# Optimization experiments

Hardware: AMD Instinct MI355X
Metric: run time of the kernel (lower is better)

The kernel has to match this reference:

```python
import jax, jax.numpy as jnp
import numpy as np

VOCAB, N_EMBD, BATCH, SEQ = 50257, 768, 8, 1024


def setup_inputs() -> dict:
    key = jax.random.key(0)
    k1, k2, k3, k4, k5 = jax.random.split(key, 5)
    data = jax.random.randint(k1, (BATCH, SEQ), 0, VOCAB, dtype=jnp.int64 if jax.config.jax_enable_x64 else jnp.int32)
    label = jax.random.randint(k2, (BATCH, SEQ), 0, VOCAB, dtype=data.dtype)
    wte = jax.random.normal(k3, (VOCAB, N_EMBD), dtype=jnp.float32) * 0.02
    wpe = jax.random.normal(k4, (SEQ, N_EMBD), dtype=jnp.float32) * 0.02
    W = jax.random.normal(k5, (VOCAB, N_EMBD), dtype=jnp.float32) * 0.02
    return {"data": data, "label": label, "wte": wte, "wpe": wpe, "W": W}


def reference(data, label, wte, wpe, W):
    # token + position embeddings: [B,S,D]
    x = wte[data] + wpe[None, :, :]
    # tanh-approx GELU (matches nn.GELU(approximate='tanh'))
    x = jax.nn.gelu(x, approximate=True)
    # vocab projection (no bias): [B,S,V]
    logits = jnp.einsum('bsd,vd->bsv', x, W)
    logits2d = logits.reshape(BATCH * SEQ, VOCAB)
    labels1d = label.reshape(BATCH * SEQ)
    logp = jax.nn.log_softmax(logits2d, axis=-1)
    nll = -jnp.take_along_axis(logp, labels1d[:, None], axis=-1)[:, 0]
    return jnp.mean(nll)
```

## Files before the change

kernel.cpp:

```cpp
#include <hip/hip_runtime.h>
#include <hip/hip_bf16.h>
#include <cmath>

#define BATCH   8
#define SEQ     1024
#define ROWS    8192
#define DIM     768
#define VOCAB   50257
#define VPAD    50304
#define NVB     393
#define NMB     64

typedef __attribute__((ext_vector_type(8))) short bf16x8;
typedef __attribute__((ext_vector_type(4))) float f32x4;

__device__ __forceinline__ float b2f(ushort u) {
    return __uint_as_float(((unsigned int)u) << 16);
}

__device__ __forceinline__ ushort f2b(float f) {
    unsigned int u = __float_as_uint(f);
    u += 0x7FFFu + ((u >> 16) & 1u);
    return (ushort)(u >> 16);
}

__device__ __forceinline__ float gelu_tanh(float x) {
    const float c = 0.7978845608028654f;
    float t = c * (x + 0.044715f * x * x * x);
    return 0.5f * x * (1.0f + tanhf(t));
}

__device__ __forceinline__ void async16(const void* g, void* l) {
    __builtin_amdgcn_global_load_lds((const __attribute__((address_space(1))) void*)g,
                                     (__attribute__((address_space(3))) void*)l,
                                     16, 0, 0);
}

__global__ void convert_w(const float* __restrict__ W, ushort* __restrict__ Wb) {
    const size_t NQ  = (size_t)VPAD  * DIM / 4;
    const size_t NVQ = (size_t)VOCAB * DIM / 4;
    for (size_t q = (size_t)blockIdx.x * blockDim.x + threadIdx.x; q < NQ;
         q += (size_t)gridDim.x * blockDim.x) {
        ushort4 o;
        if (q < NVQ) {
            float4 f = ((const float4*)W)[q];
            o.x = f2b(f.x); o.y = f2b(f.y); o.z = f2b(f.z); o.w = f2b(f.w);
        } else {
            o.x = 0; o.y = 0; o.z = 0; o.w = 0;
        }
        ((ushort4*)Wb)[q] = o;
    }
}

__global__ void build_x(const int* __restrict__ data, const float* __restrict__ wte,
                        const float* __restrict__ wpe, ushort* __restrict__ Xb) {
    const int row = blockIdx.x;
    const int s   = row & (SEQ - 1);
    const int tok = data[row];
    const int t   = threadIdx.x;
    float4 a = ((const float4*)(wte + (size_t)tok * DIM))[t];
    float4 p = ((const float4*)(wpe + (size_t)s   * DIM))[t];
    ushort4 o;
    o.x = f2b(gelu_tanh(a.x + p.x));
    o.y = f2b(gelu_tanh(a.y + p.y));
    o.z = f2b(gelu_tanh(a.z + p.z));
    o.w = f2b(gelu_tanh(a.w + p.w));
    ((ushort4*)Xb)[(size_t)row * (DIM / 4) + t] = o;
}

__global__ __launch_bounds__(256) void gemm_partial(
    const ushort* __restrict__ Xb, const ushort* __restrict__ Wb,
    float2* __restrict__ parts)
{
    __shared__ ushort lA[128 * 32];
    __shared__ ushort lB[128 * 32];
    __shared__ float2 red[128][2];

    const int bid = blockIdx.x;
    const int swz = (bid & 7) * 3144 + (bid >> 3);
    const int bm = swz & 63;
    const int bn = swz >> 6;
    const int tid = threadIdx.x;
    const int w = tid >> 6, l = tid & 63;
    const int wr = w >> 1, wc = w & 1;
    const int row0 = bm << 7, col0 = bn << 7;

    f32x4 acc[4][4] = {};

    const int srow = (w << 5) + (l >> 2);
    const int scol = (l & 3) << 3;
    const ushort* gA = Xb + (size_t)(row0 + srow) * DIM + scol;
    const ushort* gB = Wb + (size_t)(col0 + srow) * DIM + scol;
    ushort* sA = &lA[(w << 5) * 32];
    ushort* sB = &lB[(w << 5) * 32];

    const int lrow = l & 15, lk = (l >> 4) << 3;
    const ushort* pa = &lA[(wr * 64 + lrow) * 32 + lk];
    const ushort* pb = &lB[(wc * 64 + lrow) * 32 + lk];

    for (int k0 = 0; k0 < DIM; k0 += 32) {
        async16(gA + k0,            sA);
        async16(gA + k0 + 16 * DIM, sA + 16 * 32);
        async16(gB + k0,            sB);
        async16(gB + k0 + 16 * DIM, sB + 16 * 32);
        __syncthreads();

        bf16x8 af[4], bg[4];
        #pragma unroll
        for (int m = 0; m < 4; m++) af[m] = *(const bf16x8*)(pa + m * 16 * 32);
        #pragma unroll
        for (int n = 0; n < 4; n++) bg[n] = *(const bf16x8*)(pb + n * 16 * 32);

        #pragma unroll
        for (int m = 0; m < 4; m++)
            #pragma unroll
            for (int n = 0; n < 4; n++)
                acc[m][n] = __builtin_amdgcn_mfma_f32_16x16x32_bf16(
                    af[m], bg[n], acc[m][n], 0, 0, 0);
        __syncthreads();
    }

    const int qr = l >> 4, lc = l & 15;
    #pragma unroll
    for (int m = 0; m < 4; m++) {
        #pragma unroll
        for (int j = 0; j < 4; j++) {
            const int rloc = wr * 64 + m * 16 + qr * 4 + j;
            float vals[4];
            float vmax = -INFINITY;
            #pragma unroll
            for (int n = 0; n < 4; n++) {
                const int v = col0 + wc * 64 + n * 16 + lc;
                float x = acc[m][n][j];
                if (v >= VOCAB) x = -INFINITY;
                vals[n] = x;
                vmax = fmaxf(vmax, x);
            }
            #pragma unroll
            for (int off = 1; off < 16; off <<= 1)
                vmax = fmaxf(vmax, __shfl_xor(vmax, off, 64));
            float s = 0.f;
            #pragma unroll
            for (int n = 0; n < 4; n++)
                s += __expf(vals[n] - vmax);
            #pragma unroll
            for (int off = 1; off < 16; off <<= 1)
                s += __shfl_xor(s, off, 64);
            if (lc == 0) { red[rloc][wc].x = vmax; red[rloc][wc].y = s; }
        }
    }
    __syncthreads();
    if (tid < 128) {
        float2 a = red[tid][0], b = red[tid][1];
        float M = fmaxf(a.x, b.x);
        float S = a.y * __expf(a.x - M) + b.y * __expf(b.x - M);
        parts[(size_t)(row0 + tid) * NVB + bn] = make_float2(M, S);
    }
}

__global__ void finalize_k(const ushort* __restrict__ Xb, const ushort* __restrict__ Wb,
                           const int* __restrict__ label, const float2* __restrict__ parts,
                           float* __restrict__ losses) {
    const int r = blockIdx.x;
    const int l = threadIdx.x;
    const int tok = label[r];

    float dot = 0.f;
    const ushort4* xr = (const ushort4*)(Xb + (size_t)r   * DIM);
    const ushort4* wv = (const ushort4*)(Wb + (size_t)tok * DIM);
    for (int q = l; q < DIM / 4; q += 64) {
        ushort4 a = xr[q], b = wv[q];
        dot += b2f(a.x) * b2f(b.x) + b2f(a.y) * b2f(b.y)
             + b2f(a.z) * b2f(b.z) + b2f(a.w) * b2f(b.w);
    }
    #pragma unroll
    for (int off = 1; off < 64; off <<= 1) dot += __shfl_xor(dot, off, 64);

    float M = -INFINITY, S = 0.f;
    for (int p = l; p < NVB; p += 64) {
        float2 e = parts[(size_t)r * NVB + p];
        float nm = fmaxf(M, e.x);
        S = S * __expf(M - nm) + e.y * __expf(e.x - nm);
        M = nm;
    }
    #pragma unroll
    for (int off = 1; off < 64; off <<= 1) {
        float Mo = __shfl_xor(M, off, 64);
        float So = __shfl_xor(S, off, 64);
        float nm = fmaxf(M, Mo);
        S = S * __expf(M - nm) + So * __expf(Mo - nm);
        M = nm;
    }
    if (l == 0) losses[r] = M + logf(S) - dot;
}

__global__ void reduce_loss(const float* __restrict__ losses, float* __restrict__ out) {
    __shared__ float sh[256];
    float s = 0.f;
    for (int i = threadIdx.x; i < ROWS; i += 256) s += losses[i];
    sh[threadIdx.x] = s;
    __syncthreads();
    for (int st = 128; st > 0; st >>= 1) {
        if (threadIdx.x < st) sh[threadIdx.x] += sh[threadIdx.x + st];
        __syncthreads();
    }
    if (threadIdx.x == 0) out[0] = sh[0] * (1.0f / (float)ROWS);
}

extern "C" void kernel_launch(void* const* d_in, const int* in_sizes, int n_in,
                              void* d_out, int out_size, void* d_ws, size_t ws_size,
                              hipStream_t stream) {
    const int*   data  = (const int*)d_in[0];
    const int*   label = (const int*)d_in[1];
    const float* wte   = (const float*)d_in[2];
    const float* wpe   = (const float*)d_in[3];
    const float* W     = (const float*)d_in[4];
    float*       out   = (float*)d_out;

    char* ws = (char*)d_ws;
    ushort* Wb    = (ushort*)ws;
    ushort* Xb    = (ushort*)(ws + (size_t)VPAD * DIM * 2);
    float2* parts = (float2*)(ws + (size_t)VPAD * DIM * 2
                                 + (size_t)ROWS * DIM * 2);
    float* losses = (float*)(ws + (size_t)VPAD * DIM * 2
                                + (size_t)ROWS * DIM * 2
                                + (size_t)ROWS * NVB * 8);

    convert_w<<<2048, 256, 0, stream>>>(W, Wb);
    build_x<<<ROWS, DIM / 4, 0, stream>>>(data, wte, wpe, Xb);
    gemm_partial<<<NMB * NVB, 256, 0, stream>>>(Xb, Wb, parts);
    finalize_k<<<ROWS, 64, 0, stream>>>(Xb, Wb, label, parts, losses);
    reduce_loss<<<1, 256, 0, stream>>>(losses, out);
}
```

Before: 1.228 ms.

## Use 256x256 GEMM tiles with 4-stage async LDS pipeline and swizzled LDS

Grows the fused logits/softmax GEMM tile from 128x128 to 256x256 with 512 threads (8 waves, each 128x64). A 4-slot ring of LDS buffers is filled by async global-to-LDS loads three stages ahead, with explicit vmcnt waits and one barrier per k-step. An XOR swizzle on the LDS layout avoids bank conflicts, and s_setprio raises wave priority around the MFMA block. The goal is to hide load latency and raise arithmetic intensity, at the cost of more registers (32 accumulators per lane) and 128KB of LDS per block, which limits occupancy.

Result: faster. 1.084 ms (-11.7%).

```diff
diff --git a/kernel.cpp b/kernel.cpp
--- a/kernel.cpp
+++ b/kernel.cpp
@@ -7,9 +7,12 @@
 #define ROWS    8192
 #define DIM     768
 #define VOCAB   50257
-#define VPAD    50304
-#define NVB     393
-#define NMB     64
+#define VPAD    50432
+#define NVB     197
+#define NMB     32
+#define BK      32
+#define NT      24
+#define SLOT_B  32768
 
 typedef __attribute__((ext_vector_type(8))) short bf16x8;
 typedef __attribute__((ext_vector_type(4))) float f32x4;
@@ -68,64 +71,100 @@
     ((ushort4*)Xb)[(size_t)row * (DIM / 4) + t] = o;
 }
 
-__global__ __launch_bounds__(256) void gemm_partial(
+__global__ __launch_bounds__(512, 2) void gemm_partial(
     const ushort* __restrict__ Xb, const ushort* __restrict__ Wb,
     float2* __restrict__ parts)
 {
-    __shared__ ushort lA[128 * 32];
-    __shared__ ushort lB[128 * 32];
-    __shared__ float2 red[128][2];
+    __shared__ ushort tiles[4 * SLOT_B / 2];
+    char* smemc = (char*)tiles;
 
     const int bid = blockIdx.x;
-    const int swz = (bid & 7) * 3144 + (bid >> 3);
-    const int bm = swz & 63;
-    const int bn = swz >> 6;
+    const int xcd = bid & 7, idx = bid >> 3;
+    const int bm = xcd * 4 + (idx & 3);
+    const int bn = idx >> 2;
+    const int row0 = bm << 8, col0 = bn << 8;
+
     const int tid = threadIdx.x;
     const int w = tid >> 6, l = tid & 63;
-    const int wr = w >> 1, wc = w & 1;
-    const int row0 = bm << 7, col0 = bn << 7;
-
-    f32x4 acc[4][4] = {};
-
-    const int srow = (w << 5) + (l >> 2);
-    const int scol = (l & 3) << 3;
-    const ushort* gA = Xb + (size_t)(row0 + srow) * DIM + scol;
-    const ushort* gB = Wb + (size_t)(col0 + srow) * DIM + scol;
-    ushort* sA = &lA[(w << 5) * 32];
-    ushort* sB = &lB[(w << 5) * 32];
-
-    const int lrow = l & 15, lk = (l >> 4) << 3;
-    const ushort* pa = &lA[(wr * 64 + lrow) * 32 + lk];
-    const ushort* pb = &lB[(wc * 64 + lrow) * 32 + lk];
-
-    for (int k0 = 0; k0 < DIM; k0 += 32) {
-        async16(gA + k0,            sA);
-        async16(gA + k0 + 16 * DIM, sA + 16 * 32);
-        async16(gB + k0,            sB);
-        async16(gB + k0 + 16 * DIM, sB + 16 * 32);
-        __syncthreads();
-
-        bf16x8 af[4], bg[4];
-        #pragma unroll
-        for (int m = 0; m < 4; m++) af[m] = *(const bf16x8*)(pa + m * 16 * 32);
-        #pragma unroll
-        for (int n = 0; n < 4; n++) bg[n] = *(const bf16x8*)(pb + n * 16 * 32);
-
-        #pragma unroll
-        for (int m = 0; m < 4; m++)
-            #pragma unroll
-            for (int n = 0; n < 4; n++)
-                acc[m][n] = __builtin_amdgcn_mfma_f32_16x16x32_bf16(
-                    af[m], bg[n], acc[m][n], 0, 0, 0);
-        __syncthreads();
-    }
+    const int wr = w >> 2, wc = w & 3;
+
+    const int rstage = w * 16 + (l >> 2);
+    const int cswz   = ((l & 3) ^ ((l >> 3) & 3)) << 3;
+    const ushort* gA0 = Xb + (size_t)(row0 + rstage) * DIM + cswz;
+    const ushort* gA1 = gA0 + (size_t)128 * DIM;
+    const ushort* gB0 = Wb + (size_t)(col0 + rstage) * DIM + cswz;
+    const ushort* gB1 = gB0 + (size_t)128 * DIM;
+    char* ldsA = smemc + w * 1024;
+    char* ldsB = smemc + 16384 + w * 1024;
+
+    const int lrow = l & 15, cexp = l >> 4;
+    const int swzs = (lrow >> 1) & 3;
+    const int aoff = (wr * 128 + lrow) * 64 + ((cexp ^ swzs) << 4);
+    const int boff = 16384 + (wc * 64 + lrow) * 64 + ((cexp ^ swzs) << 4);
+
+    f32x4 acc[8][4] = {};
+
+#define GL(t, s) do {                                         \
+        const int koff_ = (t) * BK;                           \
+        async16(gA0 + koff_, ldsA + (s) * SLOT_B);            \
+        async16(gA1 + koff_, ldsA + (s) * SLOT_B + 8192);     \
+        async16(gB0 + koff_, ldsB + (s) * SLOT_B);            \
+        async16(gB1 + koff_, ldsB + (s) * SLOT_B + 8192);     \
+    } while (0)
+
+#define COMPUTE(t) do {                                                       \
+        const char* sb_ = smemc + ((t) & 3) * SLOT_B;                         \
+        bf16x8 af_[8], bg_[4];                                                \
+        _Pragma("unroll")                                                     \
+        for (int m_ = 0; m_ < 8; m_++)                                        \
+            af_[m_] = *(const bf16x8*)(sb_ + aoff + m_ * 1024);               \
+        _Pragma("unroll")                                                     \
+        for (int n_ = 0; n_ < 4; n_++)                                        \
+            bg_[n_] = *(const bf16x8*)(sb_ + boff + n_ * 1024);               \
+        __builtin_amdgcn_s_setprio(1);                                        \
+        _Pragma("unroll")                                                     \
+        for (int m_ = 0; m_ < 8; m_++)                                        \
+            _Pragma("unroll")                                                 \
+            for (int n_ = 0; n_ < 4; n_++)                                    \
+                acc[m_][n_] = __builtin_amdgcn_mfma_f32_16x16x32_bf16(        \
+                    af_[m_], bg_[n_], acc[m_][n_], 0, 0, 0);                  \
+        __builtin_amdgcn_s_setprio(0);                                        \
+    } while (0)
+
+    GL(0, 0); GL(1, 1); GL(2, 2);
+    asm volatile("s_waitcnt vmcnt(8)" ::: "memory");
+    __builtin_amdgcn_s_barrier();
+    asm volatile("" ::: "memory");
+
+    for (int t = 0; t < NT - 3; ++t) {
+        GL(t + 3, (t + 3) & 3);
+        COMPUTE(t);
+        asm volatile("s_waitcnt vmcnt(8)" ::: "memory");
+        __builtin_amdgcn_s_barrier();
+        asm volatile("" ::: "memory");
+    }
+    COMPUTE(21);
+    asm volatile("s_waitcnt vmcnt(4)" ::: "memory");
+    __builtin_amdgcn_s_barrier();
+    asm volatile("" ::: "memory");
+    COMPUTE(22);
+    asm volatile("s_waitcnt vmcnt(0)" ::: "memory");
+    __builtin_amdgcn_s_barrier();
+    asm volatile("" ::: "memory");
+    COMPUTE(23);
+
+#undef GL
+#undef COMPUTE
+
+    __syncthreads();
+    float2 (*red)[4] = (float2(*)[4])smemc;
 
     const int qr = l >> 4, lc = l & 15;
     #pragma unroll
-    for (int m = 0; m < 4; m++) {
+    for (int m = 0; m < 8; m++) {
         #pragma unroll
         for (int j = 0; j < 4; j++) {
-            const int rloc = wr * 64 + m * 16 + qr * 4 + j;
+            const int rloc = wr * 128 + m * 16 + qr * 4 + j;
             float vals[4];
             float vmax = -INFINITY;
             #pragma unroll
@@ -142,7 +181,7 @@
             float s = 0.f;
             #pragma unroll
             for (int n = 0; n < 4; n++)
-                s += __expf(vals[n] - vmax);
+                s += (vals[n] == -INFINITY) ? 0.f : __expf(vals[n] - vmax);
             #pragma unroll
             for (int off = 1; off < 16; off <<= 1)
                 s += __shfl_xor(s, off, 64);
@@ -150,10 +189,15 @@
         }
     }
     __syncthreads();
-    if (tid < 128) {
-        float2 a = red[tid][0], b = red[tid][1];
-        float M = fmaxf(a.x, b.x);
-        float S = a.y * __expf(a.x - M) + b.y * __expf(b.x - M);
+    if (tid < 256) {
+        float M = -INFINITY, S = 0.f;
+        #pragma unroll
+        for (int q = 0; q < 4; q++) {
+            float2 e = red[tid][q];
+            float nm = fmaxf(M, e.x);
+            S = S * __expf(M - nm) + e.y * __expf(e.x - nm);
+            M = nm;
+        }
         parts[(size_t)(row0 + tid) * NVB + bn] = make_float2(M, S);
     }
 }
@@ -228,7 +272,7 @@
 
     convert_w<<<2048, 256, 0, stream>>>(W, Wb);
     build_x<<<ROWS, DIM / 4, 0, stream>>>(data, wte, wpe, Xb);
-    gemm_partial<<<NMB * NVB, 256, 0, stream>>>(Xb, Wb, parts);
+    gemm_partial<<<NMB * NVB, 512, 0, stream>>>(Xb, Wb, parts);
     finalize_k<<<ROWS, 64, 0, stream>>>(Xb, Wb, label, parts, losses);
     reduce_loss<<<1, 256, 0, stream>>>(losses, out);
 }
```
